# Performance work log

Measured on AMD Instinct MI355X. Metric: run time of the kernel, lower is better.

The kernel has to match this reference:

```python
import jax, jax.numpy as jnp
import numpy as np

B, T, C = 4, 2048, 768
H, N = 12, 64
N_LAYER, LAYER_ID = 12, 1
EPS_GN = 0.00064


def setup_inputs():
    key = jax.random.key(0)
    ks = jax.random.split(key, 20)
    r01 = LAYER_ID / (N_LAYER - 1)
    r10 = 1.0 - LAYER_ID / N_LAYER
    ddd = (np.arange(C, dtype=np.float64) / C)[None, None, :]

    def lam(p, off=0.0):
        return jnp.asarray(1.0 - np.power(ddd, p) - off, dtype=jnp.float32)

    decay = -7.0 + 5.0 * (np.arange(C, dtype=np.float64) / (C - 1)) ** (0.85 + r01 ** 0.5)

    def rn(i, shape, scale):
        return scale * jax.random.normal(ks[i], shape, jnp.float32)

    s = 1.0 / C ** 0.5
    return {
        "x": jax.random.normal(ks[0], (B, T, C), jnp.float32),
        "v_first": jax.random.normal(ks[1], (B, T, C), jnp.float32),
        "lambda_r": lam(0.2 * r10), "lambda_w": lam(0.9 * r10),
        "lambda_k": lam(0.9 * r10, 0.4 * r01), "lambda_v": lam(0.4 * r10, 0.6 * r01),
        "lambda_a": lam(0.9 * r10), "lambda_g": lam(0.2 * r10),
        "w_miu": jnp.asarray(decay[None, None, :] + 0.5, jnp.float32),
        "w_A": rn(2, (C, 64), 0.02), "w_B": rn(3, (64, C), 0.02),
        "a_miu": jnp.zeros((1, 1, C), jnp.float32),
        "a_A": rn(4, (C, 64), 0.02), "a_B": rn(5, (64, C), 0.02),
        "v_miu": jnp.ones((1, 1, C), jnp.float32),
        "v_A": rn(6, (C, 64), 0.02), "v_B": rn(7, (64, C), 0.02),
        "g_A": rn(8, (C, 128), 0.02), "g_B": rn(9, (128, C), 0.02),
        "k_k": 0.85 * jnp.ones((1, 1, C), jnp.float32),
        "k_a": jnp.ones((1, 1, C), jnp.float32),
        "r_k": rn(10, (H, N), 0.02),
        "W_r": jax.random.uniform(ks[11], (C, C), jnp.float32, -0.5 * s, 0.5 * s),
        "W_k": jax.random.uniform(ks[12], (C, C), jnp.float32, -0.05 * s, 0.05 * s),
        "W_v": jax.random.uniform(ks[13], (C, C), jnp.float32, -0.5 * s, 0.5 * s),
        "W_o": rn(14, (C, C), 0.02),
        "ln_w": jnp.ones((C,), jnp.float32), "ln_b": jnp.zeros((C,), jnp.float32),
    }


def _wkv7(r, w, k, v, z, b):
    # r,w,k,v,z,b: (B,T,H,N). RWKV-7 linear recurrence with per-head NxN state:
    # S_t = S_{t-1}*diag(exp(-exp(w_t))) + (S_{t-1} z_t) b_t^T + v_t k_t^T ; y_t = S_t r_t
    decay = jnp.exp(-jnp.exp(w))

    def step(S, inp):
        rt, dt, kt, vt, zt, bt = inp  # each (B,H,N)
        sa = jnp.einsum('bhij,bhj->bhi', S, zt)
        S = S * dt[:, :, None, :] + sa[..., None] * bt[:, :, None, :] + vt[..., None] * kt[:, :, None, :]
        y = jnp.einsum('bhij,bhj->bhi', S, rt)
        return S, y

    seq = tuple(jnp.moveaxis(t, 1, 0) for t in (r, decay, k, v, z, b))  # (T,B,H,N)
    S0 = jnp.zeros((r.shape[0], r.shape[2], r.shape[3], r.shape[3]), r.dtype)
    _, ys = jax.lax.scan(step, S0, seq)
    return jnp.moveaxis(ys, 0, 1)  # (B,T,H,N)


def reference(x, v_first, lambda_r, lambda_w, lambda_k, lambda_v, lambda_a, lambda_g,
              w_miu, w_A, w_B, a_miu, a_A, a_B, v_miu, v_A, v_B, g_A, g_B,
              k_k, k_a, r_k, W_r, W_k, W_v, W_o, ln_w, ln_b):
    Bb, Tt, Cc = x.shape
    # ZeroPad2d((0,0,1,-1)): shift sequence right by 1, zero at t=0
    x_shift = jnp.pad(x, ((0, 0), (1, 0), (0, 0)))[:, :-1]
    xd = x_shift - x
    r = (x + xd * lambda_r) @ W_r.T
    w = x + xd * lambda_w
    k = (x + xd * lambda_k) @ W_k.T
    v = (x + xd * lambda_v) @ W_v.T
    a_in = x + xd * lambda_a
    g_in = x + xd * lambda_g
    if LAYER_ID == 0:
        v_first = v
    else:
        v = v + (v_first - v) * jax.nn.sigmoid(v_miu + (v @ v_A) @ v_B)
    w = -jax.nn.softplus(-(w_miu + jnp.tanh(w @ w_A) @ w_B)) - 0.5
    a = jax.nn.sigmoid(a_miu + (a_in @ a_A) @ a_B)
    g = jax.nn.sigmoid(g_in @ g_A) @ g_B
    kk = (k * k_k).reshape(Bb, Tt, H, N)
    kk = kk / jnp.maximum(jnp.linalg.norm(kk, axis=-1, keepdims=True), 1e-12)
    k = k * (1 + (a - 1) * k_a)
    rh = r.reshape(Bb, Tt, H, N)
    wh = w.reshape(Bb, Tt, H, N)
    kh = k.reshape(Bb, Tt, H, N)
    vh = v.reshape(Bb, Tt, H, N)
    ah = a.reshape(Bb, Tt, H, N)
    y = _wkv7(rh, wh, kh, vh, -kk, kk * ah)  # (B,T,H,N)
    # GroupNorm over heads, eps=0.00064, biased variance (torch semantics)
    mu = y.mean(-1, keepdims=True)
    var = y.var(-1, keepdims=True)
    y = ((y - mu) / jnp.sqrt(var + EPS_GN)).reshape(Bb, Tt, Cc) * ln_w + ln_b
    y = y + ((rh * kh * r_k).sum(-1, keepdims=True) * vh).reshape(Bb, Tt, Cc)
    out = (y * g) @ W_o.T
    return (out, v_first)
```

## Files before the change

### kernel.cpp

```cpp
#include <hip/hip_runtime.h>
#include <hip/hip_bf16.h>
#include <math.h>


#define B_  4
#define T_  2048
#define C_  768
#define H_  12

typedef __attribute__((ext_vector_type(8))) short bf16x8;
typedef __attribute__((ext_vector_type(4))) float f32x4;

#define GLD16(gsrc, ldst)                                                     \
  __builtin_amdgcn_global_load_lds(                                           \
      (const __attribute__((address_space(1))) void*)(gsrc),                  \
      (__attribute__((address_space(3))) void*)(ldst), 16, 0, 0)

template <int CTRL>
static __device__ __forceinline__ float row_ror_add(float v) {
  int t = __builtin_amdgcn_update_dpp(0, __float_as_int(v), CTRL, 0xF, 0xF, true);
  return v + __int_as_float(t);
}
static __device__ __forceinline__ float row_sum16(float v) {
  v = row_ror_add<0x128>(v);
  v = row_ror_add<0x124>(v);
  v = row_ror_add<0x122>(v);
  v = row_ror_add<0x121>(v);
  return v;
}

static __device__ __forceinline__ float wave_sum64(float v) {
  v = row_sum16(v);
  v += __shfl_xor(v, 16);
  v += __shfl_xor(v, 32);
  return v;
}

static __device__ __forceinline__ short bf16b(float f) {
  __hip_bfloat16 h = __float2bfloat16(f);
  return *reinterpret_cast<short*>(&h);
}

static __device__ __forceinline__ float bf2f(short s) {
  const unsigned u = ((unsigned)(unsigned short)s) << 16;
  return __int_as_float((int)u);
}

enum { EPI_NONE = 0, EPI_TANH, EPI_WDECAY, EPI_SIGBIAS, EPI_SIGMOID, EPI_VMIX };

static __device__ __forceinline__ float apply_epi_f(int epi, float val, int n,
                                                    int gmrow, int N,
                                                    const float* bias,
                                                    const float* ex1,
                                                    const float* ex2) {
  if (epi == EPI_TANH) {
    val = tanhf(val);
  } else if (epi == EPI_WDECAY) {
    const float u = bias[n] + val;
    const float sig = 1.f / (1.f + expf(-u));
    val = expf(-0.60653065971263342f * sig);
  } else if (epi == EPI_SIGBIAS) {
    const float u = bias[n] + val;
    val = 1.f / (1.f + expf(-u));
  } else if (epi == EPI_SIGMOID) {
    val = 1.f / (1.f + expf(-val));
  } else if (epi == EPI_VMIX) {
    const float u = bias[n] + val;
    const float sg = 1.f / (1.f + expf(-u));
    const size_t off = (size_t)gmrow * N + n;
    const float v0v = ex1[off];
    const float vf = ex2[off];
    val = v0v + (vf - v0v) * sg;
  }
  return val;
}

static __device__ __forceinline__ void gemm128_tile(
    const short* __restrict__ A, const short* __restrict__ Bw,
    float* __restrict__ C, short* __restrict__ C16, int M, int N, int K,
    int bx, int by, int epi, const float* bias, const float* ex1,
    const float* ex2, short* As, short* Bs) {
  const int tid = threadIdx.x;
  const int wave = tid >> 6, lane = tid & 63;
  const int m0 = by * 128, n0 = bx * 128;
  const int wm = (wave >> 1) * 64, wn = (wave & 1) * 64;
  const int fr = lane & 15, fk = (lane >> 4) * 8;

  f32x4 acc[4][4];
#pragma unroll
  for (int i = 0; i < 4; i++)
#pragma unroll
    for (int j = 0; j < 4; j++) acc[i][j] = (f32x4){0.f, 0.f, 0.f, 0.f};

  const int srow = tid >> 2, scol = (tid & 3) * 8;
  const short* gA = A + (size_t)(m0 + srow) * K + scol;
  const short* gB = Bw + (size_t)(n0 + srow) * K + scol;
  short* lA0 = &As[wave * 512];
  short* lA1 = &As[2048 + wave * 512];
  short* lB0 = &Bs[wave * 512];
  short* lB1 = &Bs[2048 + wave * 512];

  for (int k0 = 0; k0 < K; k0 += 32) {
    GLD16(gA + k0, lA0);
    GLD16(gA + (size_t)64 * K + k0, lA1);
    GLD16(gB + k0, lB0);
    GLD16(gB + (size_t)64 * K + k0, lB1);
    __syncthreads();

    bf16x8 af[4], bf[4];
#pragma unroll
    for (int i = 0; i < 4; i++)
      af[i] = *(const bf16x8*)&As[(wm + i * 16 + fr) * 32 + fk];
#pragma unroll
    for (int j = 0; j < 4; j++)
      bf[j] = *(const bf16x8*)&Bs[(wn + j * 16 + fr) * 32 + fk];
#pragma unroll
    for (int i = 0; i < 4; i++)
#pragma unroll
      for (int j = 0; j < 4; j++)
        acc[i][j] =
            __builtin_amdgcn_mfma_f32_16x16x32_bf16(af[i], bf[j], acc[i][j], 0, 0, 0);
    __syncthreads();
  }

#pragma unroll
  for (int i = 0; i < 4; i++) {
    const int gm = m0 + wm + i * 16 + (lane >> 4) * 4;
#pragma unroll
    for (int j = 0; j < 4; j++) {
      const int gn = n0 + wn + j * 16 + fr;
#pragma unroll
      for (int rix = 0; rix < 4; rix++) {
        float val = acc[i][j][rix];
        val = apply_epi_f(epi, val, gn, gm + rix, N, bias, ex1, ex2);
        C[(size_t)(gm + rix) * N + gn] = val;
        if (C16) C16[(size_t)(gm + rix) * N + gn] = bf16b(val);
      }
    }
  }
}

static __device__ __forceinline__ void gemm64_tile(
    const short* __restrict__ A, const short* __restrict__ Bw,
    short* __restrict__ out16, int M, int N, int K, int bx, int by, int epi,
    short* As, short* Bs) {
  const int tid = threadIdx.x;
  const int wave = tid >> 6, lane = tid & 63;
  const int m0 = by * 128, n0 = bx * 64;
  const int wm = (wave >> 1) * 64, wn = (wave & 1) * 32;
  const int fr = lane & 15, fk = (lane >> 4) * 8;

  f32x4 acc[4][2];
#pragma unroll
  for (int i = 0; i < 4; i++)
#pragma unroll
    for (int j = 0; j < 2; j++) acc[i][j] = (f32x4){0.f, 0.f, 0.f, 0.f};

  const int srow = tid >> 2, scol = (tid & 3) * 8;
  const short* gA = A + (size_t)(m0 + srow) * K + scol;
  const short* gB = Bw + (size_t)(n0 + srow) * K + scol;
  short* lA0 = &As[wave * 512];
  short* lA1 = &As[2048 + wave * 512];
  short* lB0 = &Bs[wave * 512];

  for (int k0 = 0; k0 < K; k0 += 32) {
    GLD16(gA + k0, lA0);
    GLD16(gA + (size_t)64 * K + k0, lA1);
    GLD16(gB + k0, lB0);
    __syncthreads();

    bf16x8 af[4], bf[2];
#pragma unroll
    for (int i = 0; i < 4; i++)
      af[i] = *(const bf16x8*)&As[(wm + i * 16 + fr) * 32 + fk];
#pragma unroll
    for (int j = 0; j < 2; j++)
      bf[j] = *(const bf16x8*)&Bs[(wn + j * 16 + fr) * 32 + fk];
#pragma unroll
    for (int i = 0; i < 4; i++)
#pragma unroll
      for (int j = 0; j < 2; j++)
        acc[i][j] =
            __builtin_amdgcn_mfma_f32_16x16x32_bf16(af[i], bf[j], acc[i][j], 0, 0, 0);
    __syncthreads();
  }

#pragma unroll
  for (int i = 0; i < 4; i++) {
    const int gm = m0 + wm + i * 16 + (lane >> 4) * 4;
#pragma unroll
    for (int j = 0; j < 2; j++) {
      const int gn = n0 + wn + j * 16 + fr;
#pragma unroll
      for (int rix = 0; rix < 4; rix++) {
        float val = acc[i][j][rix];
        if (epi == EPI_TANH) val = tanhf(val);
        else if (epi == EPI_SIGMOID) val = 1.f / (1.f + expf(-val));
        out16[(size_t)(gm + rix) * N + gn] = bf16b(val);
      }
    }
  }
}

__global__ __launch_bounds__(256) void big3_k(
    const short* __restrict__ xr, const short* __restrict__ xk,
    const short* __restrict__ xv, const short* __restrict__ wrb,
    const short* __restrict__ wkb, const short* __restrict__ wvb,
    float* __restrict__ r_, float* __restrict__ kbuf,
    float* __restrict__ vbuf, short* __restrict__ vbuf16) {
  __shared__ short smem[2 * 128 * 32];
  const int role = blockIdx.x / 6, bx = blockIdx.x % 6;
  const short* A;
  const short* Bw;
  float* C;
  short* C16 = nullptr;
  if (role == 0) { A = xr; Bw = wrb; C = r_; }
  else if (role == 1) { A = xk; Bw = wkb; C = kbuf; }
  else { A = xv; Bw = wvb; C = vbuf; C16 = vbuf16; }
  gemm128_tile(A, Bw, C, C16, B_ * T_, C_, C_, bx, blockIdx.y, EPI_NONE,
               nullptr, nullptr, nullptr, smem, smem + 128 * 32);
}

__global__ __launch_bounds__(256) void s1x4_k(
    const short* __restrict__ xw, const short* __restrict__ xa,
    const short* __restrict__ xg, const short* __restrict__ vbuf16,
    const short* __restrict__ wAT, const short* __restrict__ aAT,
    const short* __restrict__ gAT, const short* __restrict__ vAT,
    short* __restrict__ h_w, short* __restrict__ h_a,
    short* __restrict__ h_g, short* __restrict__ h_v) {
  __shared__ short smem[128 * 32 + 64 * 32];
  const int bx = blockIdx.x;
  const short* A;
  const short* Bw;
  short* O;
  int N, tb, epi;
  if (bx == 0)      { A = xw;     Bw = wAT; O = h_w; N = 64;  tb = 0; epi = EPI_TANH; }
  else if (bx == 1) { A = xa;     Bw = aAT; O = h_a; N = 64;  tb = 0; epi = EPI_NONE; }
  else if (bx == 2) { A = xg;     Bw = gAT; O = h_g; N = 128; tb = 0; epi = EPI_SIGMOID; }
  else if (bx == 3) { A = xg;     Bw = gAT; O = h_g; N = 128; tb = 1; epi = EPI_SIGMOID; }
  else              { A = vbuf16; Bw = vAT; O = h_v; N = 64;  tb = 0; epi = EPI_NONE; }
  gemm64_tile(A, Bw, O, B_ * T_, N, C_, tb, blockIdx.y, epi, smem,
              smem + 128 * 32);
}

__global__ __launch_bounds__(256) void s2x3_k(
    const short* __restrict__ h_v, const short* __restrict__ h_w,
    const short* __restrict__ h_a, const short* __restrict__ vBT,
    const short* __restrict__ wBT, const short* __restrict__ aBT,
    float* __restrict__ vbuf, float* __restrict__ dec_, float* __restrict__ a_,
    const float* __restrict__ v_miu, const float* __restrict__ w_miu,
    const float* __restrict__ a_miu, const float* __restrict__ v_first) {
  __shared__ short smem[2 * 128 * 32];
  const int role = blockIdx.x / 6, bx = blockIdx.x % 6;
  const short* A;
  const short* Bw;
  float* C;
  const float* bias;
  const float* ex1 = nullptr;
  const float* ex2 = nullptr;
  int epi;
  if (role == 0) { A = h_v; Bw = vBT; C = vbuf; bias = v_miu; ex1 = vbuf; ex2 = v_first; epi = EPI_VMIX; }
  else if (role == 1) { A = h_w; Bw = wBT; C = dec_; bias = w_miu; epi = EPI_WDECAY; }
  else { A = h_a; Bw = aBT; C = a_; bias = a_miu; epi = EPI_SIGBIAS; }
  gemm128_tile(A, Bw, C, nullptr, B_ * T_, C_, 64, bx, blockIdx.y, epi, bias,
               ex1, ex2, smem, smem + 128 * 32);
}

__global__ __launch_bounds__(256) void outp_k(
    const short* __restrict__ ymb, const short* __restrict__ wob,
    float* __restrict__ out) {
  __shared__ short smem[2 * 128 * 32];
  gemm128_tile(ymb, wob, out, nullptr, B_ * T_, C_, C_, blockIdx.x,
               blockIdx.y, EPI_NONE, nullptr, nullptr, nullptr, smem,
               smem + 128 * 32);
}

__global__ __launch_bounds__(256) void mix6_k(
    const float* __restrict__ x, const float* __restrict__ lr,
    const float* __restrict__ lk, const float* __restrict__ lv,
    const float* __restrict__ lw, const float* __restrict__ la,
    const float* __restrict__ lg, short* __restrict__ xr,
    short* __restrict__ xk, short* __restrict__ xv, short* __restrict__ xw,
    short* __restrict__ xa, short* __restrict__ xg) {
  const int i = blockIdx.x * 256 + threadIdx.x;
  const int c4 = i % (C_ / 4);
  const int gm = i / (C_ / 4);
  const float4 xa4 = ((const float4*)x)[i];
  float4 xp = make_float4(0.f, 0.f, 0.f, 0.f);
  if ((gm % T_) != 0) xp = ((const float4*)x)[i - C_ / 4];
  const float4 dx =
      make_float4(xp.x - xa4.x, xp.y - xa4.y, xp.z - xa4.z, xp.w - xa4.w);

#define MIXOUT(dst, lam)                                                      \
  {                                                                           \
    const float4 l4 = ((const float4*)lam)[c4];                               \
    short4 o = {bf16b(fmaf(dx.x, l4.x, xa4.x)),                               \
                bf16b(fmaf(dx.y, l4.y, xa4.y)),                               \
                bf16b(fmaf(dx.z, l4.z, xa4.z)),                               \
                bf16b(fmaf(dx.w, l4.w, xa4.w))};                              \
    ((short4*)dst)[i] = o;                                                    \
  }
  MIXOUT(xr, lr);
  MIXOUT(xk, lk);
  MIXOUT(xv, lv);
  MIXOUT(xw, lw);
  MIXOUT(xa, la);
  MIXOUT(xg, lg);
#undef MIXOUT
}

__global__ __launch_bounds__(256) void wprep_k(
    const float* __restrict__ W_r, const float* __restrict__ W_k,
    const float* __restrict__ W_v, const float* __restrict__ W_o,
    const float* __restrict__ w_A, const float* __restrict__ a_A,
    const float* __restrict__ v_A, const float* __restrict__ g_A,
    const float* __restrict__ w_B, const float* __restrict__ a_B,
    const float* __restrict__ v_B, const float* __restrict__ g_B,
    short* __restrict__ wrb, short* __restrict__ wkb,
    short* __restrict__ wvb, short* __restrict__ wob,
    short* __restrict__ wAT, short* __restrict__ aAT,
    short* __restrict__ vAT, short* __restrict__ gAT,
    short* __restrict__ wBT, short* __restrict__ aBT,
    short* __restrict__ vBT, short* __restrict__ gBT) {
  const int job = blockIdx.y;
  const int WN = C_ * C_;
  if (job < 4) {
    const float* src = (job == 0) ? W_r : (job == 1) ? W_k : (job == 2) ? W_v : W_o;
    short* dst = (job == 0) ? wrb : (job == 1) ? wkb : (job == 2) ? wvb : wob;
    const int n4 = WN / 4;
    for (int i = blockIdx.x * 256 + threadIdx.x; i < n4; i += gridDim.x * 256) {
      const float4 v = ((const float4*)src)[i];
      short4 o = {bf16b(v.x), bf16b(v.y), bf16b(v.z), bf16b(v.w)};
      ((short4*)dst)[i] = o;
    }
  } else {
    const float* in;
    short* out;
    int R, Cc;
    switch (job) {
      case 4: in = w_A; out = wAT; R = C_; Cc = 64; break;
      case 5: in = a_A; out = aAT; R = C_; Cc = 64; break;
      case 6: in = v_A; out = vAT; R = C_; Cc = 64; break;
      case 7: in = g_A; out = gAT; R = C_; Cc = 128; break;
      case 8: in = w_B; out = wBT; R = 64; Cc = C_; break;
      case 9: in = a_B; out = aBT; R = 64; Cc = C_; break;
      case 10: in = v_B; out = vBT; R = 64; Cc = C_; break;
      default: in = g_B; out = gBT; R = 128; Cc = C_; break;
    }
    const int n = R * Cc;
    for (int i = blockIdx.x * 256 + threadIdx.x; i < n; i += gridDim.x * 256) {
      const int r = i / Cc, c = i % Cc;
      out[(size_t)c * R + r] = bf16b(in[i]);
    }
  }
}

__global__ __launch_bounds__(256) void kkprep_k(
    const float* __restrict__ k0, const float* __restrict__ av_,
    const float* __restrict__ rr, const float* __restrict__ k_k,
    const float* __restrict__ k_a, float* __restrict__ kout,
    short* __restrict__ zb16, short* __restrict__ kr16) {
  const int tid = threadIdx.x;
  const int wv = tid >> 6, l = tid & 63;
  const int grp = l >> 4, g16 = l & 15;
  const size_t hid = (size_t)blockIdx.x * 16 + wv * 4 + grp;
  const int h = (int)(hid % H_);
  const size_t base = hid * 64 + g16 * 4;
  const int cc = h * 64 + g16 * 4;

  const float4 kv = *(const float4*)(k0 + base);
  const float4 aa = *(const float4*)(av_ + base);
  const float4 rv = *(const float4*)(rr + base);
  const float4 kkc = *(const float4*)(k_k + cc);
  const float4 kac = *(const float4*)(k_a + cc);

  const float kkx = kv.x * kkc.x, kky = kv.y * kkc.y, kkz = kv.z * kkc.z,
              kkw = kv.w * kkc.w;
  const float ssp = kkx * kkx + kky * kky + kkz * kkz + kkw * kkw;
  const float ss = row_sum16(ssp);
  const float denom = fmaxf(sqrtf(ss), 1e-12f);
  const float nx = kkx / denom, ny = kky / denom, nz = kkz / denom,
              nw = kkw / denom;

  bf16x8 zb = {bf16b(-nx), bf16b(-ny), bf16b(-nz), bf16b(-nw),
               bf16b(nx * aa.x), bf16b(ny * aa.y), bf16b(nz * aa.z),
               bf16b(nw * aa.w)};
  *(bf16x8*)(zb16 + hid * 128 + g16 * 8) = zb;

  const float knx = kv.x * (1.f + (aa.x - 1.f) * kac.x);
  const float kny = kv.y * (1.f + (aa.y - 1.f) * kac.y);
  const float knz = kv.z * (1.f + (aa.z - 1.f) * kac.z);
  const float knw = kv.w * (1.f + (aa.w - 1.f) * kac.w);
  bf16x8 kr = {bf16b(knx), bf16b(kny), bf16b(knz), bf16b(knw),
               bf16b(rv.x), bf16b(rv.y), bf16b(rv.z), bf16b(rv.w)};
  *(bf16x8*)(kr16 + hid * 128 + g16 * 8) = kr;

  *(float4*)(kout + base) = make_float4(knx, kny, knz, knw);
}

#define CH 16
#define NC (T_ / CH)
__global__ __launch_bounds__(256) void wkv7f_k(
    const float* __restrict__ dd, const float* __restrict__ vv,
    const short* __restrict__ zb16, const short* __restrict__ kr16,
    float* __restrict__ yy, const short* __restrict__ h_g,
    const short* __restrict__ gBT, float* __restrict__ g_,
    const float4* __restrict__ cpsrc, float4* __restrict__ cpdst, int n4) {
  __shared__ __align__(16) char smem[2 * 16384];
  const int blk = blockIdx.x;

  if (blk >= 240) {
    const int rb = blk - 240;
    for (int i = rb * 256 + threadIdx.x; i < n4; i += 16 * 256)
      cpdst[i] = cpsrc[i];
    return;
  }
  if (blk >= 192) {
    short* As = (short*)smem;
    short* Bs = As + 128 * 32;
    const int rb = blk - 192;
    for (int it = 0; it < 8; ++it) {
      const int tile = rb + it * 48;
      gemm128_tile(h_g, gBT, g_, nullptr, B_ * T_, C_, 128, tile % 6,
                   tile / 6, EPI_NONE, nullptr, nullptr, nullptr, As, Bs);
    }
    return;
  }

  const int bh = blk % 48;
  const int rq = blk / 48;
  const int b = bh / H_, h = bh % H_;
  const int tid = threadIdx.x;
  const int wave = tid >> 6;
  const int l = tid & 63;
  const int l16 = l & 15;
  const int row = rq * 16 + wave * 4 + (l >> 4);
  const int cb = l16 * 4;
  const size_t btb = (size_t)b * T_;

  const size_t gf0 = (btb + wave * 4 + (l >> 4)) * C_ + h * 64 + cb;
  const size_t gp0 =
      ((btb + wave * 4 + (l >> 4)) * H_ + h) * 128 + (size_t)(l & 15) * 8;

#define STAGE(BUF, GF, GP)                                                    \
  {                                                                           \
    char* Bb = smem + (BUF)*16384;                                            \
    GLD16(dd + (GF), (float*)Bb + wave * 256);                                \
    GLD16(vv + (GF), (float*)(Bb + 4096) + wave * 256);                       \
    GLD16(zb16 + (GP), (short*)(Bb + 8192) + wave * 512);                     \
    GLD16(kr16 + (GP), (short*)(Bb + 12288) + wave * 512);                    \
  }

#define LDSTEP(S_, TL_)                                                       \
  {                                                                           \
    Wf[S_] = *(const float4*)&Lw[(TL_)*64 + cb];                              \
    Vf[S_] = Lv[(TL_)*64 + row];                                              \
    ZB[S_] = *(const bf16x8*)&Lzb[(TL_)*128 + l16 * 8];                       \
    KR[S_] = *(const bf16x8*)&Lkr[(TL_)*128 + l16 * 8];                       \
  }

#define CHUNK_BODY(CIDX)                                                      \
  {                                                                           \
    float4 Wf[3];                                                             \
    float Vf[3];                                                              \
    bf16x8 ZB[3], KR[3];                                                      \
    LDSTEP(0, 0);                                                             \
    LDSTEP(1, 1);                                                             \
    _Pragma("unroll") for (int tl = 0; tl < CH; ++tl) {                       \
      const int sl = tl % 3;                                                  \
      if (tl + 2 < CH) { LDSTEP((tl + 2) % 3, tl + 2); }                      \
      const float4 w4 = Wf[sl];                                               \
      const float vi = Vf[sl];                                                \
      const bf16x8 zb = ZB[sl], kr = KR[sl];                                  \
      const float z0 = bf2f(zb[0]), z1 = bf2f(zb[1]), z2 = bf2f(zb[2]),       \
                  z3 = bf2f(zb[3]);                                           \
      const float b0 = bf2f(zb[4]), b1 = bf2f(zb[5]), b2 = bf2f(zb[6]),       \
                  b3 = bf2f(zb[7]);                                           \
      const float k0 = bf2f(kr[0]), k1 = bf2f(kr[1]), k2 = bf2f(kr[2]),       \
                  k3 = bf2f(kr[3]);                                           \
      const float r0 = bf2f(kr[4]), r1 = bf2f(kr[5]), r2 = bf2f(kr[6]),       \
                  r3 = bf2f(kr[7]);                                           \
      float sa = fmaf(S1, z1, S0 * z0) + fmaf(S3, z3, S2 * z2);               \
      sa = row_sum16(sa);                                                     \
      S0 = fmaf(S0, w4.x, fmaf(sa, b0, vi * k0));                             \
      S1 = fmaf(S1, w4.y, fmaf(sa, b1, vi * k1));                             \
      S2 = fmaf(S2, w4.z, fmaf(sa, b2, vi * k2));                             \
      S3 = fmaf(S3, w4.w, fmaf(sa, b3, vi * k3));                             \
      float yp = fmaf(S1, r1, S0 * r0) + fmaf(S3, r3, S2 * r2);               \
      yp = row_sum16(yp);                                                     \
      if (l16 == 0) yy[ybase + (size_t)((CIDX)*CH + tl) * C_] = yp;           \
    }                                                                         \
  }

  STAGE(0, gf0, gp0);
  __syncthreads();

  float S0 = 0.f, S1 = 0.f, S2 = 0.f, S3 = 0.f;
  size_t gf = gf0 + (size_t)CH * C_;
  size_t gp = gp0 + (size_t)CH * H_ * 128;
  const size_t ybase = btb * C_ + h * 64 + row;

  for (int c = 0; c < NC; c += 2) {
    STAGE(1, gf, gp);
    gf += (size_t)CH * C_;
    gp += (size_t)CH * H_ * 128;
    {
      const float* Lw = (const float*)(smem);
      const float* Lv = (const float*)(smem + 4096);
      const short* Lzb = (const short*)(smem + 8192);
      const short* Lkr = (const short*)(smem + 12288);
      CHUNK_BODY(c)
    }
    __syncthreads();
    if (c + 2 < NC) STAGE(0, gf, gp);
    gf += (size_t)CH * C_;
    gp += (size_t)CH * H_ * 128;
    {
      const float* Lw = (const float*)(smem + 16384);
      const float* Lv = (const float*)(smem + 16384 + 4096);
      const short* Lzb = (const short*)(smem + 16384 + 8192);
      const short* Lkr = (const short*)(smem + 16384 + 12288);
      CHUNK_BODY(c + 1)
    }
    __syncthreads();
  }
#undef STAGE
#undef LDSTEP
#undef CHUNK_BODY
}

__global__ __launch_bounds__(256) void gn_k(
    const float* __restrict__ y, const float* __restrict__ r,
    const float* __restrict__ k, const float* __restrict__ v,
    const float* __restrict__ g, const float* __restrict__ r_k,
    const float* __restrict__ ln_w, const float* __restrict__ ln_b,
    short* __restrict__ ymb) {
  const int wid = threadIdx.x >> 6;
  const int lane = threadIdx.x & 63;
  const size_t hid = (size_t)blockIdx.x * 4 + wid;
  const int h = (int)(hid % H_);
  const size_t idx = hid * 64 + lane;
  const int c = h * 64 + lane;

  const float yv = y[idx];
  const float mu = wave_sum64(yv) * (1.f / 64.f);
  const float sq = wave_sum64(yv * yv) * (1.f / 64.f);
  const float var = sq - mu * mu;
  float yn = (yv - mu) * rsqrtf(var + 0.00064f);
  yn = yn * ln_w[c] + ln_b[c];

  const float s = wave_sum64(r[idx] * k[idx] * r_k[c]);
  yn += s * v[idx];
  ymb[idx] = bf16b(yn * g[idx]);
}

extern "C" void kernel_launch(void* const* d_in, const int* in_sizes, int n_in,
                              void* d_out, int out_size, void* d_ws,
                              size_t ws_size, hipStream_t stream) {
  const float* x       = (const float*)d_in[0];
  const float* v_first = (const float*)d_in[1];
  const float* lam_r   = (const float*)d_in[2];
  const float* lam_w   = (const float*)d_in[3];
  const float* lam_k   = (const float*)d_in[4];
  const float* lam_v   = (const float*)d_in[5];
  const float* lam_a   = (const float*)d_in[6];
  const float* lam_g   = (const float*)d_in[7];
  const float* w_miu   = (const float*)d_in[8];
  const float* w_A     = (const float*)d_in[9];
  const float* w_B     = (const float*)d_in[10];
  const float* a_miu   = (const float*)d_in[11];
  const float* a_A     = (const float*)d_in[12];
  const float* a_B     = (const float*)d_in[13];
  const float* v_miu   = (const float*)d_in[14];
  const float* v_A     = (const float*)d_in[15];
  const float* v_B     = (const float*)d_in[16];
  const float* g_A     = (const float*)d_in[17];
  const float* g_B     = (const float*)d_in[18];
  const float* k_k     = (const float*)d_in[19];
  const float* k_a     = (const float*)d_in[20];
  const float* r_k     = (const float*)d_in[21];
  const float* W_r     = (const float*)d_in[22];
  const float* W_k     = (const float*)d_in[23];
  const float* W_v     = (const float*)d_in[24];
  const float* W_o     = (const float*)d_in[25];
  const float* ln_w    = (const float*)d_in[26];
  const float* ln_b    = (const float*)d_in[27];

  const int M = B_ * T_;
  const size_t S = (size_t)M * C_;

  float* ws   = (float*)d_ws;
  float* r_   = ws + 0 * S;
  float* kbuf = ws + 1 * S;
  float* vbuf = ws + 2 * S;
  float* dec_ = ws + 3 * S;
  float* a_   = ws + 4 * S;
  float* g_   = ws + 5 * S;
  float* z_   = ws + 6 * S;
  float* bb_  = ws + 7 * S;
  float* h_   = ws + 8 * S;
  short* wb   = (short*)(h_ + (size_t)M * 128);
  float* out  = (float*)d_out;

  const int WN = C_ * C_;
  short* wrb = wb + 0 * (size_t)WN;
  short* wkb = wb + 1 * (size_t)WN;
  short* wvb = wb + 2 * (size_t)WN;
  short* wob = wb + 3 * (size_t)WN;
  short* wAT = wb + 4 * (size_t)WN;
  short* aAT = wAT + (size_t)C_ * 64;
  short* vAT = aAT + (size_t)C_ * 64;
  short* gAT = vAT + (size_t)C_ * 64;
  short* wBT = gAT + (size_t)C_ * 128;
  short* aBT = wBT + (size_t)C_ * 64;
  short* vBT = aBT + (size_t)C_ * 64;
  short* gBT = vBT + (size_t)C_ * 64;

  short* xr  = (short*)dec_;
  short* xk  = (short*)a_;
  short* xv  = (short*)g_;
  short* xw  = (short*)z_;
  short* xa  = (short*)z_ + S;
  short* xg  = (short*)bb_;
  short* vbuf16 = (short*)bb_ + S;
  short* h_w = (short*)h_;
  short* h_a = h_w + (size_t)M * 64;
  short* h_g = h_a + (size_t)M * 64;
  short* h_v = (short*)g_;
  short* zb16 = (short*)z_;
  short* kr16 = (short*)bb_;
  short* ymb = (short*)z_;

  {
    dim3 blk(256), grid(576, 12);
    hipLaunchKernelGGL(wprep_k, grid, blk, 0, stream, W_r, W_k, W_v, W_o,
                       w_A, a_A, v_A, g_A, w_B, a_B, v_B, g_B, wrb, wkb, wvb,
                       wob, wAT, aAT, vAT, gAT, wBT, aBT, vBT, gBT);
  }
  {
    dim3 blk(256), grid((int)(S / 4 / 256));
    hipLaunchKernelGGL(mix6_k, grid, blk, 0, stream, x, lam_r, lam_k, lam_v,
                       lam_w, lam_a, lam_g, xr, xk, xv, xw, xa, xg);
  }
  {
    dim3 blk(256), grid(18, M / 128);
    hipLaunchKernelGGL(big3_k, grid, blk, 0, stream, xr, xk, xv, wrb, wkb,
                       wvb, r_, kbuf, vbuf, vbuf16);
  }
  {
    dim3 blk(256), grid(5, M / 128);
    hipLaunchKernelGGL(s1x4_k, grid, blk, 0, stream, xw, xa, xg, vbuf16, wAT,
                       aAT, gAT, vAT, h_w, h_a, h_g, h_v);
  }
  {
    dim3 blk(256), grid(18, M / 128);
    hipLaunchKernelGGL(s2x3_k, grid, blk, 0, stream, h_v, h_w, h_a, vBT, wBT,
                       aBT, vbuf, dec_, a_, v_miu, w_miu, a_miu, v_first);
  }
  {
    dim3 grid((B_ * T_ * H_) / 16), blk(256);
    hipLaunchKernelGGL(kkprep_k, grid, blk, 0, stream, kbuf, a_, r_, k_k,
                       k_a, kbuf, zb16, kr16);
  }
  {
    dim3 grid(256), blk(256);
    hipLaunchKernelGGL(wkv7f_k, grid, blk, 0, stream, dec_, vbuf, zb16, kr16,
                       a_, h_g, gBT, g_, (const float4*)v_first,
                       (float4*)(out + S), (int)(S / 4));
  }
  {
    dim3 grid((B_ * T_ * H_) / 4), blk(256);
    hipLaunchKernelGGL(gn_k, grid, blk, 0, stream, a_, r_, kbuf, vbuf, g_, r_k,
                       ln_w, ln_b, ymb);
  }
  {
    dim3 blk(256), grid(C_ / 128, M / 128);
    hipLaunchKernelGGL(outp_k, grid, blk, 0, stream, ymb, wob, out);
  }
}
```

Before: 741.0 us.

## Process WKV recurrence two timesteps at a time using precomputed pair dot products

Adds a pairdot_k kernel that precomputes eight per-head dot products for each pair of consecutive timesteps. The scan in wkv7f_k then advances the state two steps per iteration, which halves the serial chain of cross-lane reductions at the cost of more arithmetic per step and an extra kernel with its own memory traffic. The group-norm kernel is also reworked so each 16-lane group handles one head with float4 loads instead of a full wave per head. The algebraic rewrite changes floating-point ordering and relies on an extra workspace region placed after the weights.

```diff
diff --git a/kernel.cpp b/kernel.cpp
--- a/kernel.cpp
+++ b/kernel.cpp
@@ -28,7 +28,6 @@
   v = row_ror_add<0x121>(v);
   return v;
 }
-
 static __device__ __forceinline__ float wave_sum64(float v) {
   v = row_sum16(v);
   v += __shfl_xor(v, 16);
@@ -40,7 +39,6 @@
   __hip_bfloat16 h = __float2bfloat16(f);
   return *reinterpret_cast<short*>(&h);
 }
-
 static __device__ __forceinline__ float bf2f(short s) {
   const unsigned u = ((unsigned)(unsigned short)s) << 16;
   return __int_as_float((int)u);
@@ -398,14 +396,68 @@
   *(float4*)(kout + base) = make_float4(knx, kny, knz, knw);
 }
 
+__global__ __launch_bounds__(256) void pairdot_k(
+    const short* __restrict__ zb16, const short* __restrict__ kr16,
+    const float* __restrict__ dec_, float* __restrict__ pd) {
+  const int tid = threadIdx.x;
+  const int wv = tid >> 6, l = tid & 63;
+  const int grp = l >> 4, g16 = l & 15;
+  const size_t gid = (size_t)blockIdx.x * 16 + wv * 4 + grp;
+  const int pair = (int)(gid & 1023);
+  const int bh = (int)(gid >> 10);
+  const int b = bh / H_, h = bh % H_;
+  const size_t t0 = (size_t)b * T_ + pair * 2;
+  const size_t t1 = t0 + 1;
+
+  const bf16x8 zb0 = *(const bf16x8*)(zb16 + (t0 * H_ + h) * 128 + g16 * 8);
+  const bf16x8 zb1 = *(const bf16x8*)(zb16 + (t1 * H_ + h) * 128 + g16 * 8);
+  const bf16x8 kr0 = *(const bf16x8*)(kr16 + (t0 * H_ + h) * 128 + g16 * 8);
+  const bf16x8 kr1 = *(const bf16x8*)(kr16 + (t1 * H_ + h) * 128 + g16 * 8);
+  const float4 w1 = *(const float4*)(dec_ + t1 * C_ + h * 64 + g16 * 4);
+
+  float z[4], bb[4], zp[4], bp[4], k[4], r[4], kp[4], rp[4];
+#pragma unroll
+  for (int j = 0; j < 4; j++) {
+    z[j] = bf2f(zb0[j]);  bb[j] = bf2f(zb0[j + 4]);
+    zp[j] = bf2f(zb1[j]); bp[j] = bf2f(zb1[j + 4]);
+    k[j] = bf2f(kr0[j]);  r[j] = bf2f(kr0[j + 4]);
+    kp[j] = bf2f(kr1[j]); rp[j] = bf2f(kr1[j + 4]);
+  }
+  const float w1a[4] = {w1.x, w1.y, w1.z, w1.w};
+
+  float p1 = 0, p2 = 0, p3 = 0, p4 = 0, p5 = 0, p6 = 0, p7 = 0, p8 = 0;
+#pragma unroll
+  for (int j = 0; j < 4; j++) {
+    const float wr = w1a[j] * rp[j];
+    p1 = fmaf(bb[j], zp[j], p1);
+    p2 = fmaf(k[j], zp[j], p2);
+    p3 = fmaf(k[j], r[j], p3);
+    p4 = fmaf(bb[j], r[j], p4);
+    p5 = fmaf(k[j], wr, p5);
+    p6 = fmaf(bp[j], rp[j], p6);
+    p7 = fmaf(bb[j], wr, p7);
+    p8 = fmaf(kp[j], rp[j], p8);
+  }
+  const float d1 = row_sum16(p1), d2 = row_sum16(p2), d3 = row_sum16(p3),
+              d4 = row_sum16(p4), d5 = row_sum16(p5), d6 = row_sum16(p6),
+              d7 = row_sum16(p7), d8 = row_sum16(p8);
+
+  if (g16 == 0) {
+    float* o = pd + gid * 8;
+    *(float4*)(o) = make_float4(d1, d2, d3, d4);
+    *(float4*)(o + 4) = make_float4(d5, d6, d7, d8);
+  }
+}
+
 #define CH 16
 #define NC (T_ / CH)
 __global__ __launch_bounds__(256) void wkv7f_k(
     const float* __restrict__ dd, const float* __restrict__ vv,
     const short* __restrict__ zb16, const short* __restrict__ kr16,
-    float* __restrict__ yy, const short* __restrict__ h_g,
-    const short* __restrict__ gBT, float* __restrict__ g_,
-    const float4* __restrict__ cpsrc, float4* __restrict__ cpdst, int n4) {
+    const float* __restrict__ pd, float* __restrict__ yy,
+    const short* __restrict__ h_g, const short* __restrict__ gBT,
+    float* __restrict__ g_, const float4* __restrict__ cpsrc,
+    float4* __restrict__ cpdst, int n4) {
   __shared__ __align__(16) char smem[2 * 16384];
   const int blk = blockIdx.x;
 
@@ -441,6 +493,7 @@
   const size_t gf0 = (btb + wave * 4 + (l >> 4)) * C_ + h * 64 + cb;
   const size_t gp0 =
       ((btb + wave * 4 + (l >> 4)) * H_ + h) * 128 + (size_t)(l & 15) * 8;
+  const float* pdbh = pd + (size_t)bh * 1024 * 8;
 
 #define STAGE(BUF, GF, GP)                                                    \
   {                                                                           \
@@ -451,44 +504,102 @@
     GLD16(kr16 + (GP), (short*)(Bb + 12288) + wave * 512);                    \
   }
 
-#define LDSTEP(S_, TL_)                                                       \
+#define PLOAD(S_, P_)                                                         \
   {                                                                           \
-    Wf[S_] = *(const float4*)&Lw[(TL_)*64 + cb];                              \
-    Vf[S_] = Lv[(TL_)*64 + row];                                              \
-    ZB[S_] = *(const bf16x8*)&Lzb[(TL_)*128 + l16 * 8];                       \
-    KR[S_] = *(const bf16x8*)&Lkr[(TL_)*128 + l16 * 8];                       \
-  }
-
-#define CHUNK_BODY(CIDX)                                                      \
+    W0[S_] = *(const float4*)&Lw[(2 * (P_)) * 64 + cb];                       \
+    W1[S_] = *(const float4*)&Lw[(2 * (P_) + 1) * 64 + cb];                   \
+    V0[S_] = Lv[(2 * (P_)) * 64 + row];                                       \
+    V1[S_] = Lv[(2 * (P_) + 1) * 64 + row];                                   \
+    ZB0[S_] = *(const bf16x8*)&Lzb[(2 * (P_)) * 128 + l16 * 8];               \
+    ZB1[S_] = *(const bf16x8*)&Lzb[(2 * (P_) + 1) * 128 + l16 * 8];           \
+    KR0[S_] = *(const bf16x8*)&Lkr[(2 * (P_)) * 128 + l16 * 8];               \
+    KR1[S_] = *(const bf16x8*)&Lkr[(2 * (P_) + 1) * 128 + l16 * 8];           \
+    DA[S_] = *(const float4*)&pdc[(P_)*8];                                    \
+    DB[S_] = *(const float4*)&pdc[(P_)*8 + 4];                                \
+  }
+
+#define PAIR_BODY(S_, P_, CIDX)                                               \
   {                                                                           \
-    float4 Wf[3];                                                             \
-    float Vf[3];                                                              \
-    bf16x8 ZB[3], KR[3];                                                      \
-    LDSTEP(0, 0);                                                             \
-    LDSTEP(1, 1);                                                             \
-    _Pragma("unroll") for (int tl = 0; tl < CH; ++tl) {                       \
-      const int sl = tl % 3;                                                  \
-      if (tl + 2 < CH) { LDSTEP((tl + 2) % 3, tl + 2); }                      \
-      const float4 w4 = Wf[sl];                                               \
-      const float vi = Vf[sl];                                                \
-      const bf16x8 zb = ZB[sl], kr = KR[sl];                                  \
-      const float z0 = bf2f(zb[0]), z1 = bf2f(zb[1]), z2 = bf2f(zb[2]),       \
-                  z3 = bf2f(zb[3]);                                           \
-      const float b0 = bf2f(zb[4]), b1 = bf2f(zb[5]), b2 = bf2f(zb[6]),       \
-                  b3 = bf2f(zb[7]);                                           \
-      const float k0 = bf2f(kr[0]), k1 = bf2f(kr[1]), k2 = bf2f(kr[2]),       \
-                  k3 = bf2f(kr[3]);                                           \
-      const float r0 = bf2f(kr[4]), r1 = bf2f(kr[5]), r2 = bf2f(kr[6]),       \
-                  r3 = bf2f(kr[7]);                                           \
-      float sa = fmaf(S1, z1, S0 * z0) + fmaf(S3, z3, S2 * z2);               \
-      sa = row_sum16(sa);                                                     \
-      S0 = fmaf(S0, w4.x, fmaf(sa, b0, vi * k0));                             \
-      S1 = fmaf(S1, w4.y, fmaf(sa, b1, vi * k1));                             \
-      S2 = fmaf(S2, w4.z, fmaf(sa, b2, vi * k2));                             \
-      S3 = fmaf(S3, w4.w, fmaf(sa, b3, vi * k3));                             \
-      float yp = fmaf(S1, r1, S0 * r0) + fmaf(S3, r3, S2 * r2);               \
-      yp = row_sum16(yp);                                                     \
-      if (l16 == 0) yy[ybase + (size_t)((CIDX)*CH + tl) * C_] = yp;           \
+    const float4 w0 = W0[S_], w1 = W1[S_], da = DA[S_], db = DB[S_];          \
+    const float v0 = V0[S_], v1 = V1[S_];                                     \
+    const bf16x8 zbt = ZB0[S_], zbp = ZB1[S_], krt = KR0[S_], krp = KR1[S_];  \
+    const float d1 = da.x, d2 = da.y, d3 = da.z, d4 = da.w;                   \
+    const float d5 = db.x, d6 = db.y, d7 = db.z, d8 = db.w;                   \
+    const float z0 = bf2f(zbt[0]), z1 = bf2f(zbt[1]), z2 = bf2f(zbt[2]),      \
+                z3 = bf2f(zbt[3]);                                            \
+    const float b0 = bf2f(zbt[4]), b1 = bf2f(zbt[5]), b2 = bf2f(zbt[6]),      \
+                b3 = bf2f(zbt[7]);                                            \
+    const float zp0 = bf2f(zbp[0]), zp1 = bf2f(zbp[1]), zp2 = bf2f(zbp[2]),   \
+                zp3 = bf2f(zbp[3]);                                           \
+    const float bp0 = bf2f(zbp[4]), bp1 = bf2f(zbp[5]), bp2 = bf2f(zbp[6]),   \
+                bp3 = bf2f(zbp[7]);                                           \
+    const float k0 = bf2f(krt[0]), k1 = bf2f(krt[1]), k2 = bf2f(krt[2]),      \
+                k3 = bf2f(krt[3]);                                            \
+    const float r0 = bf2f(krt[4]), r1 = bf2f(krt[5]), r2 = bf2f(krt[6]),      \
+                r3 = bf2f(krt[7]);                                            \
+    const float kp0 = bf2f(krp[0]), kp1 = bf2f(krp[1]), kp2 = bf2f(krp[2]),   \
+                kp3 = bf2f(krp[3]);                                           \
+    const float rp0 = bf2f(krp[4]), rp1 = bf2f(krp[5]), rp2 = bf2f(krp[6]),   \
+                rp3 = bf2f(krp[7]);                                           \
+                                   \
+    const float W20 = w0.x * w1.x, W21 = w0.y * w1.y, W22 = w0.z * w1.z,      \
+                W23 = w0.w * w1.w;                                            \
+    const float wz0 = w0.x * zp0, wz1 = w0.y * zp1, wz2 = w0.z * zp2,         \
+                wz3 = w0.w * zp3;                                             \
+    const float bw0 = b0 * w1.x, bw1 = b1 * w1.y, bw2 = b2 * w1.z,            \
+                bw3 = b3 * w1.w;                                              \
+    const float kw0 = k0 * w1.x, kw1 = k1 * w1.y, kw2 = k2 * w1.z,            \
+                kw3 = k3 * w1.w;                                              \
+    const float ra0 = fmaf(z0, d4, w0.x * r0), ra1 = fmaf(z1, d4, w0.y * r1), \
+                ra2 = fmaf(z2, d4, w0.z * r2), ra3 = fmaf(z3, d4, w0.w * r3); \
+    const float rho0 = fmaf(zp0, d6, w1.x * rp0),                             \
+                rho1 = fmaf(zp1, d6, w1.y * rp1),                             \
+                rho2 = fmaf(zp2, d6, w1.z * rp2),                             \
+                rho3 = fmaf(zp3, d6, w1.w * rp3);                             \
+    const float cb_ = fmaf(d6, d1, d7);                                       \
+    const float rb0 = fmaf(z0, cb_, w0.x * rho0),                             \
+                rb1 = fmaf(z1, cb_, w0.y * rho1),                             \
+                rb2 = fmaf(z2, cb_, w0.z * rho2),                             \
+                rb3 = fmaf(z3, cb_, w0.w * rho3);                             \
+                                    \
+    float sap = fmaf(S1, z1, S0 * z0) + fmaf(S3, z3, S2 * z2);                \
+    float sbp = fmaf(S1, wz1, S0 * wz0) + fmaf(S3, wz3, S2 * wz2);            \
+    float yap = fmaf(S1, ra1, S0 * ra0) + fmaf(S3, ra3, S2 * ra2);            \
+    float ybp = fmaf(S1, rb1, S0 * rb0) + fmaf(S3, rb3, S2 * rb2);            \
+    const float sa = row_sum16(sap);                                          \
+    const float sb = row_sum16(sbp);                                          \
+    const float ya = row_sum16(yap);                                          \
+    const float yb = row_sum16(ybp);                                          \
+                                                \
+    const float sg = fmaf(v0, d2, fmaf(sa, d1, sb));                          \
+    S0 = fmaf(S0, W20, fmaf(sa, bw0, fmaf(sg, bp0, fmaf(v0, kw0, v1 * kp0))));\
+    S1 = fmaf(S1, W21, fmaf(sa, bw1, fmaf(sg, bp1, fmaf(v0, kw1, v1 * kp1))));\
+    S2 = fmaf(S2, W22, fmaf(sa, bw2, fmaf(sg, bp2, fmaf(v0, kw2, v1 * kp2))));\
+    S3 = fmaf(S3, W23, fmaf(sa, bw3, fmaf(sg, bp3, fmaf(v0, kw3, v1 * kp3))));\
+                                                                 \
+    if (l16 == 0) {                                                           \
+      const size_t t0off = ybase + (size_t)((CIDX)*CH + 2 * (P_)) * C_;       \
+      yy[t0off] = fmaf(v0, d3, ya);                                           \
+      yy[t0off + C_] = fmaf(v0, fmaf(d6, d2, d5), fmaf(v1, d8, yb));          \
+    }                                                                         \
+  }
+
+#define CHUNK_PAIRS(BUFOFF, CIDX)                                             \
+  {                                                                           \
+    const float* Lw = (const float*)(smem + (BUFOFF));                        \
+    const float* Lv = (const float*)(smem + (BUFOFF) + 4096);                 \
+    const short* Lzb = (const short*)(smem + (BUFOFF) + 8192);                \
+    const short* Lkr = (const short*)(smem + (BUFOFF) + 12288);               \
+    const float* pdc = pdbh + (size_t)(CIDX)*8 * 8;                           \
+    float4 W0[3], W1[3], DA[3], DB[3];                                        \
+    float V0[3], V1[3];                                                       \
+    bf16x8 ZB0[3], ZB1[3], KR0[3], KR1[3];                                    \
+    PLOAD(0, 0);                                                              \
+    PLOAD(1, 1);                                                              \
+    _Pragma("unroll") for (int p = 0; p < 8; ++p) {                           \
+      const int sl = p % 3;                                                   \
+      if (p + 2 < 8) { PLOAD((p + 2) % 3, p + 2); }                           \
+      PAIR_BODY(sl, p, CIDX)                                                  \
     }                                                                         \
   }
 
@@ -504,29 +615,18 @@
     STAGE(1, gf, gp);
     gf += (size_t)CH * C_;
     gp += (size_t)CH * H_ * 128;
-    {
-      const float* Lw = (const float*)(smem);
-      const float* Lv = (const float*)(smem + 4096);
-      const short* Lzb = (const short*)(smem + 8192);
-      const short* Lkr = (const short*)(smem + 12288);
-      CHUNK_BODY(c)
-    }
+    CHUNK_PAIRS(0, c)
     __syncthreads();
     if (c + 2 < NC) STAGE(0, gf, gp);
     gf += (size_t)CH * C_;
     gp += (size_t)CH * H_ * 128;
-    {
-      const float* Lw = (const float*)(smem + 16384);
-      const float* Lv = (const float*)(smem + 16384 + 4096);
-      const short* Lzb = (const short*)(smem + 16384 + 8192);
-      const short* Lkr = (const short*)(smem + 16384 + 12288);
-      CHUNK_BODY(c + 1)
-    }
+    CHUNK_PAIRS(16384, c + 1)
     __syncthreads();
   }
 #undef STAGE
-#undef LDSTEP
-#undef CHUNK_BODY
+#undef PLOAD
+#undef PAIR_BODY
+#undef CHUNK_PAIRS
 }
 
 __global__ __launch_bounds__(256) void gn_k(
@@ -535,23 +635,38 @@
     const float* __restrict__ g, const float* __restrict__ r_k,
     const float* __restrict__ ln_w, const float* __restrict__ ln_b,
     short* __restrict__ ymb) {
-  const int wid = threadIdx.x >> 6;
-  const int lane = threadIdx.x & 63;
-  const size_t hid = (size_t)blockIdx.x * 4 + wid;
+  const int tid = threadIdx.x;
+  const int wv = tid >> 6, l = tid & 63;
+  const int grp = l >> 4, g16 = l & 15;
+  const size_t hid = (size_t)blockIdx.x * 16 + wv * 4 + grp;
   const int h = (int)(hid % H_);
-  const size_t idx = hid * 64 + lane;
-  const int c = h * 64 + lane;
-
-  const float yv = y[idx];
-  const float mu = wave_sum64(yv) * (1.f / 64.f);
-  const float sq = wave_sum64(yv * yv) * (1.f / 64.f);
-  const float var = sq - mu * mu;
-  float yn = (yv - mu) * rsqrtf(var + 0.00064f);
-  yn = yn * ln_w[c] + ln_b[c];
-
-  const float s = wave_sum64(r[idx] * k[idx] * r_k[c]);
-  yn += s * v[idx];
-  ymb[idx] = bf16b(yn * g[idx]);
+  const size_t base = hid * 64 + g16 * 4;
+  const int cc = h * 64 + g16 * 4;
+
+  const float4 y4 = *(const float4*)(y + base);
+  const float4 r4 = *(const float4*)(r + base);
+  const float4 k4 = *(const float4*)(k + base);
+  const float4 v4 = *(const float4*)(v + base);
+  const float4 g4 = *(const float4*)(g + base);
+  const float4 rk4 = *(const float4*)(r_k + cc);
+  const float4 lw4 = *(const float4*)(ln_w + cc);
+  const float4 lb4 = *(const float4*)(ln_b + cc);
+
+  const float mu =
+      row_sum16(y4.x + y4.y + y4.z + y4.w) * (1.f / 64.f);
+  const float sq =
+      row_sum16(y4.x * y4.x + y4.y * y4.y + y4.z * y4.z + y4.w * y4.w) *
+      (1.f / 64.f);
+  const float s = row_sum16(r4.x * k4.x * rk4.x + r4.y * k4.y * rk4.y +
+                            r4.z * k4.z * rk4.z + r4.w * k4.w * rk4.w);
+  const float inv = rsqrtf(sq - mu * mu + 0.00064f);
+
+  short4 o;
+  o.x = bf16b((fmaf((y4.x - mu) * inv, lw4.x, fmaf(s, v4.x, lb4.x))) * g4.x);
+  o.y = bf16b((fmaf((y4.y - mu) * inv, lw4.y, fmaf(s, v4.y, lb4.y))) * g4.y);
+  o.z = bf16b((fmaf((y4.z - mu) * inv, lw4.z, fmaf(s, v4.z, lb4.z))) * g4.z);
+  o.w = bf16b((fmaf((y4.w - mu) * inv, lw4.w, fmaf(s, v4.w, lb4.w))) * g4.w);
+  *(short4*)(ymb + base) = o;
 }
 
 extern "C" void kernel_launch(void* const* d_in, const int* in_sizes, int n_in,
@@ -615,6 +730,8 @@
   short* aBT = wBT + (size_t)C_ * 64;
   short* vBT = aBT + (size_t)C_ * 64;
   short* gBT = vBT + (size_t)C_ * 64;
+  short* wend = gBT + (size_t)C_ * 128;
+  float* pd = (float*)((((uintptr_t)wend) + 15) & ~(uintptr_t)15);
 
   short* xr  = (short*)dec_;
   short* xk  = (short*)a_;
@@ -663,13 +780,17 @@
                        k_a, kbuf, zb16, kr16);
   }
   {
+    dim3 grid(48 * 1024 / 16), blk(256);
+    hipLaunchKernelGGL(pairdot_k, grid, blk, 0, stream, zb16, kr16, dec_, pd);
+  }
+  {
     dim3 grid(256), blk(256);
     hipLaunchKernelGGL(wkv7f_k, grid, blk, 0, stream, dec_, vbuf, zb16, kr16,
-                       a_, h_g, gBT, g_, (const float4*)v_first,
+                       pd, a_, h_g, gBT, g_, (const float4*)v_first,
                        (float4*)(out + S), (int)(S / 4));
   }
   {
-    dim3 grid((B_ * T_ * H_) / 4), blk(256);
+    dim3 grid((B_ * T_ * H_) / 16), blk(256);
     hipLaunchKernelGGL(gn_k, grid, blk, 0, stream, a_, r_, kbuf, vbuf, g_, r_k,
                        ln_w, ln_b, ymb);
   }
```

Result: slower. 816.1 us (+10.1%).
